# Kernel optimization log

Measured on AMD Instinct MI355X. Metric: run time of the kernel, lower is better.

The kernel has to match this reference:

```python
import jax, jax.numpy as jnp
import numpy as np

N = 50000   # vertices
E = 25000   # hyperedges
NNZ = 400000  # incidence pairs (v, e)
D_IN = 512
D_OUT = 512  # heads * out_channels, heads=1


def setup_inputs() -> dict:
    key = jax.random.key(0)
    kx, kw, kv, ke = jax.random.split(key, 4)
    X = jax.random.normal(kx, (N, D_IN), dtype=jnp.float32)
    W = jax.random.normal(kw, (D_OUT, D_IN), dtype=jnp.float32) * 0.02  # nn.Linear weight [out,in]
    vidx = jax.random.randint(kv, (NNZ,), 0, N, dtype=jnp.int32)
    eidx = jax.random.randint(ke, (NNZ,), 0, E, dtype=jnp.int32)
    # degE = 1/|e| (hyperedge size), degV = 1/deg(v), as precomputed by hyperg
    ones = jnp.ones((NNZ,), dtype=jnp.float32)
    edge_sz = jax.ops.segment_sum(ones, eidx, num_segments=E)
    vert_dg = jax.ops.segment_sum(ones, vidx, num_segments=N)
    degE = 1.0 / jnp.maximum(edge_sz, 1.0)
    degV = 1.0 / jnp.maximum(vert_dg, 1.0)
    Wdiag = jnp.ones((E,), dtype=jnp.float32)
    return {"X": X, "W": W, "degE": degE, "degV": degV, "Wdiag": Wdiag,
            "vidx": vidx, "eidx": eidx}


def reference(X, W, degE, degV, Wdiag, vidx, eidx):
    # Dense projection: X @ W^T (nn.Linear, no bias)
    Xp = jnp.einsum('nd,od->no', X, W)                      # [N, D_OUT]
    # Stage 1: vertex -> hyperedge (first_aggr: mean via degE), weighted by Wdiag
    Xe = jax.ops.segment_sum(Xp[vidx], eidx, num_segments=E)  # [E, D_OUT]
    Xe = Xe * (degE * Wdiag)[:, None]
    # Stage 2: hyperedge -> vertex, normalized by degV
    Xv = jax.ops.segment_sum(Xe[eidx], vidx, num_segments=N)  # [N, D_OUT]
    Xv = Xv * degV[:, None]
    return Xv
```

## Files before the change

kernel.cpp:

```cpp
#include <hip/hip_runtime.h>

typedef unsigned short u16;
typedef unsigned int   u32;
typedef __attribute__((ext_vector_type(4))) float f32x4;
typedef __attribute__((ext_vector_type(4))) u32   u32x4;
typedef __attribute__((ext_vector_type(8))) __bf16 bf16x8;

constexpr int NV   = 50000;
constexpr int NE   = 25000;
constexpr int NNZp = 400000;
constexpr int D    = 512;
constexpr int MP2  = 25088;
constexpr int NBE  = 25;
constexpr int NBV  = 49;
constexpr int BPS1 = 391;
constexpr int BPS2 = 1563;

static __device__ __forceinline__ u16 f2bf(float f) {
  u32 u = __float_as_uint(f);
  u32 r = (u + 0x7fffu + ((u >> 16) & 1u)) >> 16;
  return (u16)r;
}
static __device__ __forceinline__ u32 pk2(float a, float b) {
  return (u32)f2bf(a) | ((u32)f2bf(b) << 16);
}

static __device__ __forceinline__ void gload_lds16(const u16* g, u16* l) {
  __builtin_amdgcn_global_load_lds(
      (const __attribute__((address_space(1))) u32*)g,
      (__attribute__((address_space(3))) u32*)l, 16, 0, 0);
}

__global__ void zero_kernel(int* cntE, int* cntV, int* dhistE, int* dhistV) {
  int i = blockIdx.x * 256 + threadIdx.x;
  if (i < NE) cntE[i] = 0;
  if (i < NV) cntV[i] = 0;
  if (i < 64) { dhistE[i] = 0; dhistV[i] = 0; }
}

__global__ void hist_kernel(const int* __restrict__ vidx, const int* __restrict__ eidx,
                            int* cntE, int* cntV) {
  int i = blockIdx.x * 256 + threadIdx.x;
  if (i < NNZp) {
    atomicAdd(&cntE[eidx[i]], 1);
    atomicAdd(&cntV[vidx[i]], 1);
  }
}

__global__ __launch_bounds__(256) void deghist_kernel(
    const int* __restrict__ cntE, const int* __restrict__ cntV, int* dhistE, int* dhistV) {
  __shared__ int lhE[64], lhV[64];
  int t = threadIdx.x;
  if (t < 64) { lhE[t] = 0; lhV[t] = 0; }
  __syncthreads();
  int i = blockIdx.x * 256 + t;
  if (i < NE) atomicAdd(&lhE[min(cntE[i], 63)], 1);
  if (i < NV) atomicAdd(&lhV[min(cntV[i], 63)], 1);
  __syncthreads();
  if (t < 64) { if (lhE[t]) atomicAdd(&dhistE[t], lhE[t]); }
  else if (t < 128) { int u = t - 64; if (lhV[u]) atomicAdd(&dhistV[u], lhV[u]); }
}

__global__ __launch_bounds__(256) void scan1_kernel(
    const int* __restrict__ cntE, const int* __restrict__ cntV,
    int* offE, int* offV, int* blkSum) {
  const bool isE = blockIdx.x < NBE;
  const int* cnt = isE ? cntE : cntV;
  int* off = isE ? offE : offV;
  const int len = isE ? NE : NV;
  const int t = threadIdx.x;
  const int base = (isE ? blockIdx.x : blockIdx.x - NBE) * 1024 + t * 4;
  int4 c = {0, 0, 0, 0};
  if (base + 4 <= len) c = *(const int4*)(cnt + base);
  else {
    if (base + 0 < len) c.x = cnt[base + 0];
    if (base + 1 < len) c.y = cnt[base + 1];
    if (base + 2 < len) c.z = cnt[base + 2];
    if (base + 3 < len) c.w = cnt[base + 3];
  }
  int s = c.x + c.y + c.z + c.w;
  __shared__ int sm[256];
  sm[t] = s;
  __syncthreads();
  for (int d = 1; d < 256; d <<= 1) {
    int u = (t >= d) ? sm[t - d] : 0;
    __syncthreads();
    sm[t] += u;
    __syncthreads();
  }
  int ex = sm[t] - s;
  int4 o;
  o.x = ex; o.y = o.x + c.x; o.z = o.y + c.y; o.w = o.z + c.z;
  if (base + 4 <= len) *(int4*)(off + base) = o;
  else {
    if (base + 0 < len) off[base + 0] = o.x;
    if (base + 1 < len) off[base + 1] = o.y;
    if (base + 2 < len) off[base + 2] = o.z;
    if (base + 3 < len) off[base + 3] = o.w;
  }
  if (t == 255) blkSum[blockIdx.x] = sm[255];
}

__global__ void scan2_kernel(int* blkSum, const int* __restrict__ dhistE,
                             const int* __restrict__ dhistV, int* dcurE, int* dcurV) {
  int wv = threadIdx.x >> 6, lane = threadIdx.x & 63;
  const int* s; int* d; int len;
  if (wv == 0)      { s = blkSum;       d = blkSum;       len = NBE; }
  else if (wv == 1) { s = blkSum + NBE; d = blkSum + NBE; len = NBV; }
  else if (wv == 2) { s = dhistE;       d = dcurE;        len = 64;  }
  else              { s = dhistV;       d = dcurV;        len = 64;  }
  int v = (lane < len) ? s[lane] : 0;
  int incl = v;
#pragma unroll
  for (int dd = 1; dd < 64; dd <<= 1) {
    int u = __shfl_up(incl, dd, 64);
    if (lane >= dd) incl += u;
  }
  if (lane < len) d[lane] = incl - v;
}

__global__ __launch_bounds__(256) void scan3_kernel(
    int* offE, int* offV, int* curE, int* curV, const int* __restrict__ blkSum) {
  const bool isE = blockIdx.x < NBE;
  int* off = isE ? offE : offV;
  int* cur = isE ? curE : curV;
  const int len = isE ? NE : NV;
  const int pref = blkSum[blockIdx.x];
  const int base = (isE ? blockIdx.x : blockIdx.x - NBE) * 1024 + threadIdx.x * 4;
  if (base + 4 <= len) {
    int4 o = *(int4*)(off + base);
    o.x += pref; o.y += pref; o.z += pref; o.w += pref;
    *(int4*)(off + base) = o;
    *(int4*)(cur + base) = o;
  } else {
    for (int q = 0; q < 4; q++)
      if (base + q < len) { int v = off[base + q] + pref; off[base + q] = v; cur[base + q] = v; }
  }
}

__global__ void scatter_kernel(const int* __restrict__ vidx, const int* __restrict__ eidx,
                               int* curE, int* curV, int* csr_ev, int* csr_ve) {
  int i = blockIdx.x * 256 + threadIdx.x;
  if (i < NNZp) {
    int e = eidx[i], v = vidx[i];
    csr_ev[atomicAdd(&curE[e], 1)] = v;
    csr_ve[atomicAdd(&curV[v], 1)] = e;
  }
}

__global__ __launch_bounds__(256) void degsort_kernel(
    const int* __restrict__ cntE, const int* __restrict__ offE,
    const int* __restrict__ cntV, const int* __restrict__ offV,
    const float* __restrict__ degV, int* dcurE, int* dcurV,
    int* sE_id, int* sE_off, int* sE_cnt,
    int* sV_id, int* sV_off, int* sV_cnt, float* sV_deg) {
  __shared__ int lhE[64], lhV[64], lbE[64], lbV[64];
  int t = threadIdx.x;
  if (t < 64) { lhE[t] = 0; lhV[t] = 0; }
  __syncthreads();
  int i = blockIdx.x * 256 + t;
  int bE = 0, rE = 0, bV = 0, rV = 0;
  if (i < NE) { bE = min(cntE[i], 63); rE = atomicAdd(&lhE[bE], 1); }
  if (i < NV) { bV = min(cntV[i], 63); rV = atomicAdd(&lhV[bV], 1); }
  __syncthreads();
  if (t < 64) { lbE[t] = lhE[t] ? atomicAdd(&dcurE[t], lhE[t]) : 0; }
  else if (t < 128) { int u = t - 64; lbV[u] = lhV[u] ? atomicAdd(&dcurV[u], lhV[u]) : 0; }
  __syncthreads();
  if (i < NE) {
    int r = lbE[bE] + rE;
    sE_id[r] = i; sE_off[r] = offE[i]; sE_cnt[r] = cntE[i];
  }
  if (i < NV) {
    int r = lbV[bV] + rV;
    sV_id[r] = i; sV_off[r] = offV[i]; sV_cnt[r] = cntV[i]; sV_deg[r] = degV[i];
  }
}

__global__ __launch_bounds__(256) void convert_kernel(
    const float* __restrict__ X, const float* __restrict__ W,
    u16* __restrict__ Xb, u16* __restrict__ Wb) {
  constexpr size_t NX = (size_t)NV * D;
  size_t i = ((size_t)blockIdx.x * 256 + threadIdx.x) * 8;
  const float* src;
  u16* dst;
  if (i < NX) {
    int n = (int)(i >> 9);
    int col = (int)(i & 511);
    int t = col >> 5, w = col & 31;
    src = X + i;
    dst = Xb + (size_t)t * NV * 32 + (size_t)n * 32 + w;
  } else {
    src = W + (i - NX);
    dst = Wb + (i - NX);
  }
  f32x4 a = *(const f32x4*)src;
  f32x4 b = *(const f32x4*)(src + 4);
  u32x4 p = { pk2(a[0], a[1]), pk2(a[2], a[3]), pk2(b[0], b[1]), pk2(b[2], b[3]) };
  *(u32x4*)dst = p;
}

__global__ __launch_bounds__(256) void stage1_kernel(
    const u16* __restrict__ Xb, const int* __restrict__ sE_off, const int* __restrict__ sE_cnt,
    const int* __restrict__ sE_id, const int* __restrict__ csr_ev, u16* __restrict__ XeR) {
  const int wave = threadIdx.x >> 6;
  const int lane = threadIdx.x & 63;
  const int g    = lane >> 2;
  const int c    = lane & 3;
  const int bid  = blockIdx.x;
  const int xcd  = bid & 7;
  const int tmp  = bid >> 3;
  const int phase = (tmp >= BPS1) ? 1 : 0;
  const int eg    = tmp - phase * BPS1;
  const int t     = xcd + 8 * phase;
  const int rank  = eg * 64 + wave * 16 + g;
  const u16* base = Xb + (size_t)t * NV * 32;
  int start = 0, cnt = 0, e = 0;
  if (rank < NE) {
    start = __builtin_nontemporal_load(sE_off + rank);
    cnt   = __builtin_nontemporal_load(sE_cnt + rank);
    e     = __builtin_nontemporal_load(sE_id + rank);
  }
  float acc[8] = {};
  int j0 = 0;
  for (; j0 + 4 <= cnt; j0 += 4) {
    int idx[4];
#pragma unroll
    for (int p = 0; p < 4; p++) idx[p] = __builtin_nontemporal_load(csr_ev + start + j0 + p);
    u32x4 pk[4];
#pragma unroll
    for (int p = 0; p < 4; p++) pk[p] = *(const u32x4*)(base + (size_t)idx[p] * 32 + c * 8);
#pragma unroll
    for (int p = 0; p < 4; p++)
#pragma unroll
      for (int q = 0; q < 4; q++) {
        u32 u = pk[p][q];
        acc[2 * q]     += __uint_as_float(u << 16);
        acc[2 * q + 1] += __uint_as_float(u & 0xffff0000u);
      }
  }
  for (; j0 < cnt; j0++) {
    int v = __builtin_nontemporal_load(csr_ev + start + j0);
    u32x4 p = *(const u32x4*)(base + (size_t)v * 32 + c * 8);
#pragma unroll
    for (int q = 0; q < 4; q++) {
      u32 u = p[q];
      acc[2 * q]     += __uint_as_float(u << 16);
      acc[2 * q + 1] += __uint_as_float(u & 0xffff0000u);
    }
  }
  if (rank < NE) {
    u32x4 o = { pk2(acc[0], acc[1]), pk2(acc[2], acc[3]),
                pk2(acc[4], acc[5]), pk2(acc[6], acc[7]) };
    *(u32x4*)(XeR + (size_t)e * D + t * 32 + c * 8) = o;
  }
}

__global__ __launch_bounds__(256) void gemm_kernel(const u16* __restrict__ A,
                                                   const u16* __restrict__ B,
                                                   const float* __restrict__ degE,
                                                   const float* __restrict__ Wdiag,
                                                   u16* __restrict__ C) {
  __shared__ u16 sA[128 * 32];
  __shared__ u16 sB[128 * 32];
  const int tid  = threadIdx.x;
  const int lane = tid & 63;
  const int wave = tid >> 6;
  const int bm = blockIdx.y * 128;
  const int bn = blockIdx.x * 128;
  const int wm = (wave >> 1) * 64;
  const int wn = (wave & 1) * 64;
  const int lr = lane & 15;
  const int lk = (lane >> 4) * 8;
  const int srow = lane >> 2;
  const int scol = (lane & 3) * 8;

  f32x4 acc[4][4] = {};

  for (int kt = 0; kt < D; kt += 32) {
    __syncthreads();
#pragma unroll
    for (int c = 0; c < 2; c++) {
      const int ar = wave * 16 + c * 64;
      gload_lds16(A + (size_t)(bm + ar + srow) * D + kt + scol, &sA[ar * 32]);
      gload_lds16(B + (size_t)(bn + ar + srow) * D + kt + scol, &sB[ar * 32]);
    }
    __syncthreads();

    bf16x8 af[4], bfr[4];
#pragma unroll
    for (int i = 0; i < 4; i++) af[i]  = *(const bf16x8*)&sA[(wm + i * 16 + lr) * 32 + lk];
#pragma unroll
    for (int j = 0; j < 4; j++) bfr[j] = *(const bf16x8*)&sB[(wn + j * 16 + lr) * 32 + lk];
#pragma unroll
    for (int i = 0; i < 4; i++)
#pragma unroll
      for (int j = 0; j < 4; j++)
        acc[i][j] = __builtin_amdgcn_mfma_f32_16x16x32_bf16(af[i], bfr[j], acc[i][j], 0, 0, 0);
  }

#pragma unroll
  for (int i = 0; i < 4; i++)
#pragma unroll
    for (int r = 0; r < 4; r++) {
      int row = bm + wm + i * 16 + (lane >> 4) * 4 + r;
      if (row < NE) {
        float se = degE[row] * Wdiag[row];
#pragma unroll
        for (int j = 0; j < 4; j++) {
          int col = bn + wn + lr + j * 16;
          int s = col >> 6, w = col & 63;
          C[(size_t)s * MP2 * 64 + (size_t)row * 64 + w] = f2bf(acc[i][j][r] * se);
        }
      }
    }
}

__global__ __launch_bounds__(256) void stage2_kernel(
    const u16* __restrict__ Xe2, const int* __restrict__ sV_off, const int* __restrict__ sV_cnt,
    const int* __restrict__ sV_id, const float* __restrict__ sV_deg,
    const int* __restrict__ csr_ve, float* __restrict__ out) {
  const int wave = threadIdx.x >> 6;
  const int lane = threadIdx.x & 63;
  const int g    = lane >> 3;
  const int c    = lane & 7;
  const int s    = blockIdx.x & 7;
  const int vg   = blockIdx.x >> 3;
  const int rank = vg * 32 + wave * 8 + g;
  const u16* base = Xe2 + (size_t)s * MP2 * 64;
  int start = 0, cnt = 0, v = 0;
  float dv = 0.f;
  if (rank < NV) {
    start = __builtin_nontemporal_load(sV_off + rank);
    cnt   = __builtin_nontemporal_load(sV_cnt + rank);
    v     = __builtin_nontemporal_load(sV_id + rank);
    dv    = __builtin_nontemporal_load(sV_deg + rank);
  }
  float acc[8] = {};
  int j0 = 0;
  for (; j0 + 4 <= cnt; j0 += 4) {
    int idx[4];
#pragma unroll
    for (int p = 0; p < 4; p++) idx[p] = __builtin_nontemporal_load(csr_ve + start + j0 + p);
    u32x4 pk[4];
#pragma unroll
    for (int p = 0; p < 4; p++) pk[p] = *(const u32x4*)(base + (size_t)idx[p] * 64 + c * 8);
#pragma unroll
    for (int p = 0; p < 4; p++)
#pragma unroll
      for (int q = 0; q < 4; q++) {
        u32 u = pk[p][q];
        acc[2 * q]     += __uint_as_float(u << 16);
        acc[2 * q + 1] += __uint_as_float(u & 0xffff0000u);
      }
  }
  for (; j0 < cnt; j0++) {
    int e = __builtin_nontemporal_load(csr_ve + start + j0);
    u32x4 p = *(const u32x4*)(base + (size_t)e * 64 + c * 8);
#pragma unroll
    for (int q = 0; q < 4; q++) {
      u32 u = p[q];
      acc[2 * q]     += __uint_as_float(u << 16);
      acc[2 * q + 1] += __uint_as_float(u & 0xffff0000u);
    }
  }
  if (rank < NV) {
    float* orow = out + (size_t)v * D + s * 64 + c * 8;
    f32x4 o0 = { acc[0] * dv, acc[1] * dv, acc[2] * dv, acc[3] * dv };
    f32x4 o1 = { acc[4] * dv, acc[5] * dv, acc[6] * dv, acc[7] * dv };
    *(f32x4*)orow = o0;
    *(f32x4*)(orow + 4) = o1;
  }
}

extern "C" void kernel_launch(void* const* d_in, const int* in_sizes, int n_in,
                              void* d_out, int out_size, void* d_ws, size_t ws_size,
                              hipStream_t stream) {
  const float* X     = (const float*)d_in[0];
  const float* W     = (const float*)d_in[1];
  const float* degE  = (const float*)d_in[2];
  const float* degV  = (const float*)d_in[3];
  const float* Wdiag = (const float*)d_in[4];
  const int*   vidx  = (const int*)d_in[5];
  const int*   eidx  = (const int*)d_in[6];
  float* out = (float*)d_out;

  char* p = (char*)d_ws;
  auto take = [&](size_t bytes) { char* r = p; p += (bytes + 255) & ~(size_t)255; return r; };
  u16* Xb     = (u16*)take((size_t)NV * D * 2);
  u16* Wb     = (u16*)take((size_t)D * D * 2);
  u16* XeR    = (u16*)take((size_t)MP2 * D * 2);
  u16* Xe2    = (u16*)take((size_t)MP2 * D * 2);
  int* cntE   = (int*)take((size_t)NE * 4);
  int* offE   = (int*)take((size_t)NE * 4);
  int* curE   = (int*)take((size_t)NE * 4);
  int* cntV   = (int*)take((size_t)NV * 4);
  int* offV   = (int*)take((size_t)NV * 4);
  int* curV   = (int*)take((size_t)NV * 4);
  int* csr_ev = (int*)take((size_t)NNZp * 4);
  int* csr_ve = (int*)take((size_t)NNZp * 4);
  int* blkSum = (int*)take((size_t)(NBE + NBV) * 4);
  int* dhistE = (int*)take(64 * 4);
  int* dhistV = (int*)take(64 * 4);
  int* dcurE  = (int*)take(64 * 4);
  int* dcurV  = (int*)take(64 * 4);
  int* sE_id  = (int*)take((size_t)NE * 4);
  int* sE_off = (int*)take((size_t)NE * 4);
  int* sE_cnt = (int*)take((size_t)NE * 4);
  int* sV_id  = (int*)take((size_t)NV * 4);
  int* sV_off = (int*)take((size_t)NV * 4);
  int* sV_cnt = (int*)take((size_t)NV * 4);
  float* sV_deg = (float*)take((size_t)NV * 4);

  constexpr size_t NCONV = ((size_t)NV * D + (size_t)D * D) / 8 / 256;
  constexpr int NSEG = (NV + 255) / 256;

  zero_kernel   <<<NSEG, 256, 0, stream>>>(cntE, cntV, dhistE, dhistV);
  hist_kernel   <<<(NNZp + 255) / 256, 256, 0, stream>>>(vidx, eidx, cntE, cntV);
  deghist_kernel<<<NSEG, 256, 0, stream>>>(cntE, cntV, dhistE, dhistV);
  scan1_kernel  <<<NBE + NBV, 256, 0, stream>>>(cntE, cntV, offE, offV, blkSum);
  scan2_kernel  <<<1, 256, 0, stream>>>(blkSum, dhistE, dhistV, dcurE, dcurV);
  scan3_kernel  <<<NBE + NBV, 256, 0, stream>>>(offE, offV, curE, curV, blkSum);
  scatter_kernel<<<(NNZp + 255) / 256, 256, 0, stream>>>(vidx, eidx, curE, curV, csr_ev, csr_ve);
  degsort_kernel<<<NSEG, 256, 0, stream>>>(cntE, offE, cntV, offV, degV, dcurE, dcurV,
                                           sE_id, sE_off, sE_cnt, sV_id, sV_off, sV_cnt, sV_deg);
  convert_kernel<<<NCONV, 256, 0, stream>>>(X, W, Xb, Wb);
  stage1_kernel <<<BPS1 * 16, 256, 0, stream>>>(Xb, sE_off, sE_cnt, sE_id, csr_ev, XeR);
  gemm_kernel   <<<dim3(D / 128, MP2 / 128), 256, 0, stream>>>(XeR, Wb, degE, Wdiag, Xe2);
  stage2_kernel <<<BPS2 * 8, 256, 0, stream>>>(Xe2, sV_off, sV_cnt, sV_id, sV_deg, csr_ve, out);
}
```

Measured before the change: 516.9 us.

## Pack sorted metadata into int4, widen gather batches to 16, use nontemporal stores

Packs the per-edge and per-vertex sorted metadata (id, offset, count, degree) into one 16-byte record so each gather wave does a single vector load instead of three or four scalar ones. Both gather kernels now batch 16 neighbor indices and row loads per iteration, with a masked tail batch replacing the scalar remainder loop, to keep more memory requests in flight. Intermediate and output writes switch to nontemporal stores to limit cache pollution. The masked tail still issues 16 index and row loads even when few neighbors remain, which reads past the segment into valid memory. The larger unroll also raises register pressure and may lower occupancy.

```diff
diff --git a/kernel.cpp b/kernel.cpp
--- a/kernel.cpp
+++ b/kernel.cpp
@@ -4,6 +4,7 @@
 typedef unsigned int   u32;
 typedef __attribute__((ext_vector_type(4))) float f32x4;
 typedef __attribute__((ext_vector_type(4))) u32   u32x4;
+typedef __attribute__((ext_vector_type(4))) int   i32x4;
 typedef __attribute__((ext_vector_type(8))) __bf16 bf16x8;
 
 constexpr int NV   = 50000;
@@ -152,8 +153,7 @@
     const int* __restrict__ cntE, const int* __restrict__ offE,
     const int* __restrict__ cntV, const int* __restrict__ offV,
     const float* __restrict__ degV, int* dcurE, int* dcurV,
-    int* sE_id, int* sE_off, int* sE_cnt,
-    int* sV_id, int* sV_off, int* sV_cnt, float* sV_deg) {
+    i32x4* sE_meta, i32x4* sV_meta) {
   __shared__ int lhE[64], lhV[64], lbE[64], lbV[64];
   int t = threadIdx.x;
   if (t < 64) { lhE[t] = 0; lhV[t] = 0; }
@@ -168,11 +168,13 @@
   __syncthreads();
   if (i < NE) {
     int r = lbE[bE] + rE;
-    sE_id[r] = i; sE_off[r] = offE[i]; sE_cnt[r] = cntE[i];
+    i32x4 m = { i, offE[i], cntE[i], 0 };
+    sE_meta[r] = m;
   }
   if (i < NV) {
     int r = lbV[bV] + rV;
-    sV_id[r] = i; sV_off[r] = offV[i]; sV_cnt[r] = cntV[i]; sV_deg[r] = degV[i];
+    i32x4 m = { i, offV[i], cntV[i], __float_as_int(degV[i]) };
+    sV_meta[r] = m;
   }
 }
 
@@ -196,12 +198,12 @@
   f32x4 a = *(const f32x4*)src;
   f32x4 b = *(const f32x4*)(src + 4);
   u32x4 p = { pk2(a[0], a[1]), pk2(a[2], a[3]), pk2(b[0], b[1]), pk2(b[2], b[3]) };
-  *(u32x4*)dst = p;
+  __builtin_nontemporal_store(p, (u32x4*)dst);
 }
 
 __global__ __launch_bounds__(256) void stage1_kernel(
-    const u16* __restrict__ Xb, const int* __restrict__ sE_off, const int* __restrict__ sE_cnt,
-    const int* __restrict__ sE_id, const int* __restrict__ csr_ev, u16* __restrict__ XeR) {
+    const u16* __restrict__ Xb, const i32x4* __restrict__ sE_meta,
+    const int* __restrict__ csr_ev, u16* __restrict__ XeR) {
   const int wave = threadIdx.x >> 6;
   const int lane = threadIdx.x & 63;
   const int g    = lane >> 2;
@@ -214,23 +216,22 @@
   const int t     = xcd + 8 * phase;
   const int rank  = eg * 64 + wave * 16 + g;
   const u16* base = Xb + (size_t)t * NV * 32;
-  int start = 0, cnt = 0, e = 0;
+  int e = 0, start = 0, cnt = 0;
   if (rank < NE) {
-    start = __builtin_nontemporal_load(sE_off + rank);
-    cnt   = __builtin_nontemporal_load(sE_cnt + rank);
-    e     = __builtin_nontemporal_load(sE_id + rank);
+    i32x4 m = __builtin_nontemporal_load(sE_meta + rank);
+    e = m.x; start = m.y; cnt = m.z;
   }
   float acc[8] = {};
-  int j0 = 0;
-  for (; j0 + 4 <= cnt; j0 += 4) {
-    int idx[4];
-#pragma unroll
-    for (int p = 0; p < 4; p++) idx[p] = __builtin_nontemporal_load(csr_ev + start + j0 + p);
-    u32x4 pk[4];
-#pragma unroll
-    for (int p = 0; p < 4; p++) pk[p] = *(const u32x4*)(base + (size_t)idx[p] * 32 + c * 8);
-#pragma unroll
-    for (int p = 0; p < 4; p++)
+  int b0 = 0;
+  for (; b0 + 16 <= cnt; b0 += 16) {
+    int idx[16];
+#pragma unroll
+    for (int p = 0; p < 16; p++) idx[p] = __builtin_nontemporal_load(csr_ev + start + b0 + p);
+    u32x4 pk[16];
+#pragma unroll
+    for (int p = 0; p < 16; p++) pk[p] = *(const u32x4*)(base + (size_t)idx[p] * 32 + c * 8);
+#pragma unroll
+    for (int p = 0; p < 16; p++)
 #pragma unroll
       for (int q = 0; q < 4; q++) {
         u32 u = pk[p][q];
@@ -238,20 +239,31 @@
         acc[2 * q + 1] += __uint_as_float(u & 0xffff0000u);
       }
   }
-  for (; j0 < cnt; j0++) {
-    int v = __builtin_nontemporal_load(csr_ev + start + j0);
-    u32x4 p = *(const u32x4*)(base + (size_t)v * 32 + c * 8);
-#pragma unroll
-    for (int q = 0; q < 4; q++) {
-      u32 u = p[q];
-      acc[2 * q]     += __uint_as_float(u << 16);
-      acc[2 * q + 1] += __uint_as_float(u & 0xffff0000u);
+  const int rem = cnt - b0;
+  if (rem > 0) {
+    int idx[16];
+#pragma unroll
+    for (int p = 0; p < 16; p++) {
+      int j = __builtin_nontemporal_load(csr_ev + start + b0 + p);
+      idx[p] = (p < rem) ? j : 0;
     }
+    u32x4 pk[16];
+#pragma unroll
+    for (int p = 0; p < 16; p++) pk[p] = *(const u32x4*)(base + (size_t)idx[p] * 32 + c * 8);
+#pragma unroll
+    for (int p = 0; p < 16; p++)
+      if (p < rem)
+#pragma unroll
+        for (int q = 0; q < 4; q++) {
+          u32 u = pk[p][q];
+          acc[2 * q]     += __uint_as_float(u << 16);
+          acc[2 * q + 1] += __uint_as_float(u & 0xffff0000u);
+        }
   }
   if (rank < NE) {
     u32x4 o = { pk2(acc[0], acc[1]), pk2(acc[2], acc[3]),
                 pk2(acc[4], acc[5]), pk2(acc[6], acc[7]) };
-    *(u32x4*)(XeR + (size_t)e * D + t * 32 + c * 8) = o;
+    __builtin_nontemporal_store(o, (u32x4*)(XeR + (size_t)e * D + t * 32 + c * 8));
   }
 }
 
@@ -309,15 +321,15 @@
         for (int j = 0; j < 4; j++) {
           int col = bn + wn + lr + j * 16;
           int s = col >> 6, w = col & 63;
-          C[(size_t)s * MP2 * 64 + (size_t)row * 64 + w] = f2bf(acc[i][j][r] * se);
+          __builtin_nontemporal_store(f2bf(acc[i][j][r] * se),
+                                      C + (size_t)s * MP2 * 64 + (size_t)row * 64 + w);
         }
       }
     }
 }
 
 __global__ __launch_bounds__(256) void stage2_kernel(
-    const u16* __restrict__ Xe2, const int* __restrict__ sV_off, const int* __restrict__ sV_cnt,
-    const int* __restrict__ sV_id, const float* __restrict__ sV_deg,
+    const u16* __restrict__ Xe2, const i32x4* __restrict__ sV_meta,
     const int* __restrict__ csr_ve, float* __restrict__ out) {
   const int wave = threadIdx.x >> 6;
   const int lane = threadIdx.x & 63;
@@ -327,25 +339,23 @@
   const int vg   = blockIdx.x >> 3;
   const int rank = vg * 32 + wave * 8 + g;
   const u16* base = Xe2 + (size_t)s * MP2 * 64;
-  int start = 0, cnt = 0, v = 0;
+  int v = 0, start = 0, cnt = 0;
   float dv = 0.f;
   if (rank < NV) {
-    start = __builtin_nontemporal_load(sV_off + rank);
-    cnt   = __builtin_nontemporal_load(sV_cnt + rank);
-    v     = __builtin_nontemporal_load(sV_id + rank);
-    dv    = __builtin_nontemporal_load(sV_deg + rank);
+    i32x4 m = __builtin_nontemporal_load(sV_meta + rank);
+    v = m.x; start = m.y; cnt = m.z; dv = __int_as_float(m.w);
   }
   float acc[8] = {};
-  int j0 = 0;
-  for (; j0 + 4 <= cnt; j0 += 4) {
-    int idx[4];
-#pragma unroll
-    for (int p = 0; p < 4; p++) idx[p] = __builtin_nontemporal_load(csr_ve + start + j0 + p);
-    u32x4 pk[4];
-#pragma unroll
-    for (int p = 0; p < 4; p++) pk[p] = *(const u32x4*)(base + (size_t)idx[p] * 64 + c * 8);
-#pragma unroll
-    for (int p = 0; p < 4; p++)
+  int b0 = 0;
+  for (; b0 + 16 <= cnt; b0 += 16) {
+    int idx[16];
+#pragma unroll
+    for (int p = 0; p < 16; p++) idx[p] = __builtin_nontemporal_load(csr_ve + start + b0 + p);
+    u32x4 pk[16];
+#pragma unroll
+    for (int p = 0; p < 16; p++) pk[p] = *(const u32x4*)(base + (size_t)idx[p] * 64 + c * 8);
+#pragma unroll
+    for (int p = 0; p < 16; p++)
 #pragma unroll
       for (int q = 0; q < 4; q++) {
         u32 u = pk[p][q];
@@ -353,22 +363,33 @@
         acc[2 * q + 1] += __uint_as_float(u & 0xffff0000u);
       }
   }
-  for (; j0 < cnt; j0++) {
-    int e = __builtin_nontemporal_load(csr_ve + start + j0);
-    u32x4 p = *(const u32x4*)(base + (size_t)e * 64 + c * 8);
-#pragma unroll
-    for (int q = 0; q < 4; q++) {
-      u32 u = p[q];
-      acc[2 * q]     += __uint_as_float(u << 16);
-      acc[2 * q + 1] += __uint_as_float(u & 0xffff0000u);
+  const int rem = cnt - b0;
+  if (rem > 0) {
+    int idx[16];
+#pragma unroll
+    for (int p = 0; p < 16; p++) {
+      int j = __builtin_nontemporal_load(csr_ve + start + b0 + p);
+      idx[p] = (p < rem) ? j : 0;
     }
+    u32x4 pk[16];
+#pragma unroll
+    for (int p = 0; p < 16; p++) pk[p] = *(const u32x4*)(base + (size_t)idx[p] * 64 + c * 8);
+#pragma unroll
+    for (int p = 0; p < 16; p++)
+      if (p < rem)
+#pragma unroll
+        for (int q = 0; q < 4; q++) {
+          u32 u = pk[p][q];
+          acc[2 * q]     += __uint_as_float(u << 16);
+          acc[2 * q + 1] += __uint_as_float(u & 0xffff0000u);
+        }
   }
   if (rank < NV) {
     float* orow = out + (size_t)v * D + s * 64 + c * 8;
     f32x4 o0 = { acc[0] * dv, acc[1] * dv, acc[2] * dv, acc[3] * dv };
     f32x4 o1 = { acc[4] * dv, acc[5] * dv, acc[6] * dv, acc[7] * dv };
-    *(f32x4*)orow = o0;
-    *(f32x4*)(orow + 4) = o1;
+    __builtin_nontemporal_store(o0, (f32x4*)orow);
+    __builtin_nontemporal_store(o1, (f32x4*)(orow + 4));
   }
 }
 
@@ -403,13 +424,8 @@
   int* dhistV = (int*)take(64 * 4);
   int* dcurE  = (int*)take(64 * 4);
   int* dcurV  = (int*)take(64 * 4);
-  int* sE_id  = (int*)take((size_t)NE * 4);
-  int* sE_off = (int*)take((size_t)NE * 4);
-  int* sE_cnt = (int*)take((size_t)NE * 4);
-  int* sV_id  = (int*)take((size_t)NV * 4);
-  int* sV_off = (int*)take((size_t)NV * 4);
-  int* sV_cnt = (int*)take((size_t)NV * 4);
-  float* sV_deg = (float*)take((size_t)NV * 4);
+  i32x4* sE_meta = (i32x4*)take((size_t)NE * 16);
+  i32x4* sV_meta = (i32x4*)take((size_t)NV * 16);
 
   constexpr size_t NCONV = ((size_t)NV * D + (size_t)D * D) / 8 / 256;
   constexpr int NSEG = (NV + 255) / 256;
@@ -422,9 +438,9 @@
   scan3_kernel  <<<NBE + NBV, 256, 0, stream>>>(offE, offV, curE, curV, blkSum);
   scatter_kernel<<<(NNZp + 255) / 256, 256, 0, stream>>>(vidx, eidx, curE, curV, csr_ev, csr_ve);
   degsort_kernel<<<NSEG, 256, 0, stream>>>(cntE, offE, cntV, offV, degV, dcurE, dcurV,
-                                           sE_id, sE_off, sE_cnt, sV_id, sV_off, sV_cnt, sV_deg);
+                                           sE_meta, sV_meta);
   convert_kernel<<<NCONV, 256, 0, stream>>>(X, W, Xb, Wb);
-  stage1_kernel <<<BPS1 * 16, 256, 0, stream>>>(Xb, sE_off, sE_cnt, sE_id, csr_ev, XeR);
+  stage1_kernel <<<BPS1 * 16, 256, 0, stream>>>(Xb, sE_meta, csr_ev, XeR);
   gemm_kernel   <<<dim3(D / 128, MP2 / 128), 256, 0, stream>>>(XeR, Wb, degE, Wdiag, Xe2);
-  stage2_kernel <<<BPS2 * 8, 256, 0, stream>>>(Xe2, sV_off, sV_cnt, sV_id, sV_deg, csr_ve, out);
-}
+  stage2_kernel <<<BPS2 * 8, 256, 0, stream>>>(Xe2, sV_meta, csr_ve, out);
+}
```

Result: no change. 527.1 us (+2.0%).
